# Optimization experiments

Measured on AMD Instinct MI355X. Metric: run time of the kernel, lower is better.

## Reference

```python
import jax, jax.numpy as jnp
import numpy as np

IN_CH, OUT_CH, KS = 64, 128, 3
GRID, DEG = 8, 3
STRIDE, PAD = 1, 1
SIZE = IN_CH * KS * KS            # 576
NCOEF = GRID + DEG                # 11
GRID_RANGE = (-1.0, 1.0)


def _xavier_uniform(key, shape):
    fan_out, fan_in = shape
    a = float(np.sqrt(6.0 / (fan_in + fan_out)))
    return jax.random.uniform(key, shape, minval=-a, maxval=a, dtype=jnp.float32)


def setup_inputs() -> dict:
    key = jax.random.key(0)
    k1, k2, k3 = jax.random.split(key, 3)
    x = jax.random.normal(k1, (8, IN_CH, 32, 32), dtype=jnp.float32)
    # non-trainable knot grid, one row per unfolded feature
    knots = jnp.tile(jnp.linspace(GRID_RANGE[0], GRID_RANGE[1], GRID + 1, dtype=jnp.float32)[None, :], (SIZE, 1))
    coeff = 0.1 * jax.random.normal(k2, (OUT_CH, SIZE, NCOEF), dtype=jnp.float32)
    base_weights = _xavier_uniform(k3, (OUT_CH, SIZE))
    spline_weights = jnp.ones((OUT_CH, SIZE), dtype=jnp.float32)
    return {"x": x, "knots": knots, "coeff": coeff,
            "base_weights": base_weights, "spline_weights": spline_weights}


def bspline_basis(x, grid, k):
    # x: (S, P) evaluation points; grid: (S, G+1) knots. Returns (S, G+k, P).
    h = (grid[:, -1:] - grid[:, :1]) / (grid.shape[1] - 1)
    left = grid[:, :1] - h * jnp.arange(k, 0, -1, dtype=x.dtype)
    right = grid[:, -1:] + h * jnp.arange(1, k + 1, dtype=x.dtype)
    g = jnp.concatenate([left, grid, right], axis=1)  # (S, G+1+2k)
    xe = x[:, None, :]
    B = ((xe >= g[:, :-1, None]) & (xe < g[:, 1:, None])).astype(x.dtype)
    for d in range(1, k + 1):  # de Boor recursion over fixed degree
        B = ((xe - g[:, :-(d + 1), None]) / (g[:, d:-1, None] - g[:, :-(d + 1), None]) * B[:, :-1]
             + (g[:, d + 1:, None] - xe) / (g[:, d + 1:, None] - g[:, 1:-d, None]) * B[:, 1:])
    return B


def _unfold(x):
    # torch F.unfold with channel-major (c, kh, kw) feature ordering
    N, C, H, W = x.shape
    xp = jnp.pad(x, ((0, 0), (0, 0), (PAD, PAD), (PAD, PAD)))
    Hp = (H + 2 * PAD - KS) // STRIDE + 1
    Wp = (W + 2 * PAD - KS) // STRIDE + 1
    patches = jnp.stack([xp[:, :, i:i + STRIDE * Hp:STRIDE, j:j + STRIDE * Wp:STRIDE]
                         for i in range(KS) for j in range(KS)], axis=2)  # (N, C, KS*KS, Hp, Wp)
    L = Hp * Wp
    u = patches.reshape(N, SIZE, L)              # (N, size, L)
    u = jnp.transpose(u, (1, 0, 2)).reshape(SIZE, N * L)  # (size, N*L), col = n*L + l
    return u, Hp, Wp


def reference(x, knots, coeff, base_weights, spline_weights):
    N = x.shape[0]
    u, Hp, Wp = _unfold(x)                                   # (size, P)
    base = base_weights @ jax.nn.silu(u)                     # (Cout, P)
    B = bspline_basis(u, knots, DEG)                         # (size, ncoef, P)
    eff = spline_weights[:, :, None] * coeff                 # (Cout, size, ncoef)
    spl = jnp.einsum('csj,sjp->cp', eff, B)                  # (Cout, P)
    out = (base + spl).reshape(OUT_CH, N, Hp, Wp)
    return jnp.transpose(out, (1, 0, 2, 3))                  # (N, Cout, Hp, Wp)
```

## Files before the change

### kernel.cpp

```cpp
#include <hip/hip_runtime.h>


typedef __attribute__((ext_vector_type(8))) short bf16x8;
typedef __attribute__((ext_vector_type(4))) float f32x4;
typedef __attribute__((ext_vector_type(16))) float f32x16;
typedef __attribute__((ext_vector_type(4))) unsigned short u16x4;

#define WSWZ_BYTES 1769472
#define PART_OFF   WSWZ_BYTES

__device__ __forceinline__ short f2bf(float f) {
    union { float f; unsigned u; } c; c.f = f;
    unsigned r = c.u + 0x7fffu + ((c.u >> 16) & 1u);
    return (short)(r >> 16);
}
__device__ __forceinline__ float bf2f(unsigned short u) {
    union { unsigned u; float f; } c; c.u = ((unsigned)u) << 16;
    return c.f;
}

__global__ void kan_weights(const float* __restrict__ coeff,
                            const float* __restrict__ basew,
                            const float* __restrict__ splw,
                            short* __restrict__ Wswz) {
    __shared__ float coeffL[6336];
    __shared__ float basewL[576];
    __shared__ float splwL[576];
    const int co = blockIdx.x;
    const int t  = threadIdx.x;
    const float* crow = coeff + co * 6336;
    for (int i = t; i < 6336; i += 256) coeffL[i] = crow[i];
    for (int i = t; i < 576; i += 256) {
        basewL[i] = basew[co * 576 + i];
        splwL[i]  = splw[co * 576 + i];
    }
    __syncthreads();
    const int cb = co >> 5, lm = co & 31;
    for (int c = t; c < 864; c += 256) {
        int kk16 = c >> 1, kh = c & 1;
        int f  = kk16 / 36;
        int rm = kk16 - f * 36;
        int tap = rm >> 2, q = rm & 3;
        bf16x8 pack;
#pragma unroll
        for (int j = 0; j < 8; ++j) {
            int ci = q * 16 + kh * 8 + j;
            int s  = ci * 9 + tap;
            float v = (f == 0) ? basewL[s] : splwL[s] * coeffL[s * 11 + (f - 1)];
            pack[j] = f2bf(v);
        }
        *(bf16x8*)(Wswz + (size_t)((kk16 * 4 + cb) * 64 + kh * 32 + lm) * 8) = pack;
    }
}

__global__ __launch_bounds__(256, 3)
void kan_gemm(const float* __restrict__ x,
              const short* __restrict__ Wswz,
              float* __restrict__ part) {
    __shared__ unsigned short xs[4 * 64 * 34];
    __shared__ short Bs[2 * 8704];

    const int t  = threadIdx.x;
    const int w  = t >> 6;
    const int l  = t & 63;
    const int ln = l & 31;
    const int kh = l >> 5;

    const int fg    = blockIdx.x >> 7;
    const int ptile = blockIdx.x & 127;
    const int n     = ptile >> 4;
    const int y0    = (ptile & 15) << 1;

#pragma unroll
    for (int it = 0; it < 8; ++it) {
        int cg = t + it * 256;
        int rr = cg >> 9, ci = (cg >> 3) & 63, q = cg & 7;
        int y  = y0 - 1 + rr;
        f32x4 v = {0.f, 0.f, 0.f, 0.f};
        if (y >= 0 && y < 32)
            v = *(const f32x4*)(x + (((n * 64 + ci) * 32 + y) * 32 + q * 4));
        u16x4 p;
        p.x = (unsigned short)f2bf(v.x); p.y = (unsigned short)f2bf(v.y);
        p.z = (unsigned short)f2bf(v.z); p.w = (unsigned short)f2bf(v.w);
        *(u16x4*)&xs[(rr * 64 + ci) * 34 + q * 4] = p;
    }
    __syncthreads();

    const int f0 = fg * 2;
    for (int it = t; it < 1088; it += 256) {
        int rr  = it / 272;
        int rem = it - rr * 272;
        int xp = rem >> 3, cch = rem & 7, c0 = cch << 3;
        bool interior = (xp >= 1 && xp <= 32);
        bf16x8 packs[2];
#pragma unroll
        for (int j = 0; j < 8; ++j) {
            float v = interior ? bf2f(xs[(rr * 64 + c0 + j) * 34 + (xp - 1)]) : 0.f;
            float tt = 4.f * v + 7.f;
            int   i0 = -100;
            float b0 = 0.f, b1 = 0.f, b2 = 0.f, b3 = 0.f;
            if (tt >= 0.f && tt < 14.f) {
                i0 = (int)tt;
                float fr  = tt - (float)i0;
                float omf = 1.f - fr;
                float fr2 = fr * fr, fr3 = fr2 * fr;
                b0 = omf * omf * omf * (1.f / 6.f);
                b1 = (3.f * fr3 - 6.f * fr2 + 4.f) * (1.f / 6.f);
                b2 = (-3.f * fr3 + 3.f * fr2 + 3.f * fr + 1.f) * (1.f / 6.f);
                b3 = fr3 * (1.f / 6.f);
            }
            float silu = 0.f;
            if (f0 == 0)
                silu = v * __builtin_amdgcn_rcpf(1.f + __expf(-v));
#pragma unroll
            for (int p = 0; p < 2; ++p) {
                int f = f0 + p;
                float val;
                if (f == 0) val = silu;
                else {
                    int jj = f - 1;
                    val = 0.f;
                    val = (jj == i0 - 3) ? b0 : val;
                    val = (jj == i0 - 2) ? b1 : val;
                    val = (jj == i0 - 1) ? b2 : val;
                    val = (jj == i0    ) ? b3 : val;
                }
                packs[p][j] = f2bf(val);
            }
        }
        int pix = rr * 34 + xp;
        int swz = (cch ^ (pix & 7)) << 3;
#pragma unroll
        for (int p = 0; p < 2; ++p)
            *(bf16x8*)&Bs[p * 8704 + pix * 64 + swz] = packs[p];
    }
    __syncthreads();

    f32x16 acc[2];
#pragma unroll
    for (int pb = 0; pb < 2; ++pb)
#pragma unroll
        for (int r = 0; r < 16; ++r)
            acc[pb][r] = 0.f;

    const short* Abase = Wswz + (size_t)w * 512 + (size_t)l * 8;
#pragma unroll 1
    for (int p = 0; p < 2; ++p) {
        const short* B0 = Bs + p * 8704;
        const int kbase = (f0 + p) * 36;
#pragma unroll
        for (int q = 0; q < 4; ++q) {
#pragma unroll
            for (int dx = 0; dx < 3; ++dx) {
                bf16x8 a0 = *(const bf16x8*)(Abase + (size_t)(kbase + (0 * 3 + dx) * 4 + q) * 2048);
                bf16x8 a1 = *(const bf16x8*)(Abase + (size_t)(kbase + (1 * 3 + dx) * 4 + q) * 2048);
                bf16x8 a2 = *(const bf16x8*)(Abase + (size_t)(kbase + (2 * 3 + dx) * 4 + q) * 2048);
                const int c = q * 2 + kh;
                bf16x8 b0, b1, b2, b3;
                {
                    int pix0 = 0 * 34 + ln + dx;
                    int pix1 = 1 * 34 + ln + dx;
                    int pix2 = 2 * 34 + ln + dx;
                    int pix3 = 3 * 34 + ln + dx;
                    b0 = *(const bf16x8*)&B0[pix0 * 64 + ((c ^ (pix0 & 7)) << 3)];
                    b1 = *(const bf16x8*)&B0[pix1 * 64 + ((c ^ (pix1 & 7)) << 3)];
                    b2 = *(const bf16x8*)&B0[pix2 * 64 + ((c ^ (pix2 & 7)) << 3)];
                    b3 = *(const bf16x8*)&B0[pix3 * 64 + ((c ^ (pix3 & 7)) << 3)];
                }
                acc[0] = __builtin_amdgcn_mfma_f32_32x32x16_bf16(a0, b0, acc[0], 0, 0, 0);
                acc[1] = __builtin_amdgcn_mfma_f32_32x32x16_bf16(a0, b1, acc[1], 0, 0, 0);
                acc[0] = __builtin_amdgcn_mfma_f32_32x32x16_bf16(a1, b1, acc[0], 0, 0, 0);
                acc[1] = __builtin_amdgcn_mfma_f32_32x32x16_bf16(a1, b2, acc[1], 0, 0, 0);
                acc[0] = __builtin_amdgcn_mfma_f32_32x32x16_bf16(a2, b2, acc[0], 0, 0, 0);
                acc[1] = __builtin_amdgcn_mfma_f32_32x32x16_bf16(a2, b3, acc[1], 0, 0, 0);
            }
        }
    }

    float* dst = part + (size_t)fg * 1048576;
#pragma unroll
    for (int pb = 0; pb < 2; ++pb) {
        int y = y0 + pb;
#pragma unroll
        for (int r = 0; r < 16; ++r) {
            int row = (r & 3) + 8 * (r >> 2) + 4 * kh;
            int co  = w * 32 + row;
            dst[((size_t)(n * 128 + co) * 32 + y) * 32 + ln] = acc[pb][r];
        }
    }
}

__global__ void kan_reduce(const float* __restrict__ part,
                           float* __restrict__ out) {
    const int r = blockIdx.x;
    const int p = r & 127;
    const int i = r >> 7;
    const int n  = p >> 4;
    const int yp = p & 15;
    const int c  = i * 256 + threadIdx.x;
    const int co = c >> 4;
    const int rem = c & 15;
    const int yy = rem >> 3, xq = rem & 7;
    const size_t idx = ((size_t)(n * 128 + co) * 32 + yp * 2 + yy) * 8 + xq;
    f32x4 a = ((const f32x4*)part)[idx];
#pragma unroll
    for (int s = 1; s < 6; ++s)
        a += ((const f32x4*)(part + (size_t)s * 1048576))[idx];
    ((f32x4*)out)[idx] = a;
}

extern "C" void kernel_launch(void* const* d_in, const int* in_sizes, int n_in,
                              void* d_out, int out_size, void* d_ws, size_t ws_size,
                              hipStream_t stream) {
    const float* x     = (const float*)d_in[0];
    const float* coeff = (const float*)d_in[2];
    const float* basew = (const float*)d_in[3];
    const float* splw  = (const float*)d_in[4];
    float* out = (float*)d_out;

    short* Wswz = (short*)d_ws;
    float* part = (float*)((char*)d_ws + PART_OFF);

    kan_weights<<<128, 256, 0, stream>>>(coeff, basew, splw, Wswz);
    kan_gemm<<<768, 256, 0, stream>>>(x, Wswz, part);
    kan_reduce<<<1024, 256, 0, stream>>>(part, out);
}
```

Measured before the change: 111.7 us.

## Precompute basis tiles once in prep kernel and stream them to LDS in GEMM

Moves the unfold, SiLU and B-spline basis evaluation out of the GEMM into the prep kernel. There it is computed once per pixel tile for all 12 feature groups and written to a ~27MB bf16 workspace, in the same swizzled layout the GEMM's LDS expects. Before, each of the 6 feature-group blocks recomputed the x tile and its basis. The GEMM now only copies its precomputed tile into LDS with global_load_lds, drops the xs buffer, and raises launch bounds to 4 waves per SIMD. The cost is extra global write and read traffic for the Phi buffer, plus a prep kernel with fewer, heavier blocks.

```diff
diff --git a/kernel.cpp b/kernel.cpp
--- a/kernel.cpp
+++ b/kernel.cpp
@@ -7,7 +7,9 @@
 typedef __attribute__((ext_vector_type(4))) unsigned short u16x4;
 
 #define WSWZ_BYTES 1769472
-#define PART_OFF   WSWZ_BYTES
+#define PHI_OFF    WSWZ_BYTES
+#define PHI_BYTES  26738688
+#define PART_OFF   (PHI_OFF + PHI_BYTES)
 
 __device__ __forceinline__ short f2bf(float f) {
     union { float f; unsigned u; } c; c.f = f;
@@ -19,45 +21,114 @@
     return c.f;
 }
 
-__global__ void kan_weights(const float* __restrict__ coeff,
-                            const float* __restrict__ basew,
-                            const float* __restrict__ splw,
-                            short* __restrict__ Wswz) {
+__global__ void kan_prep(const float* __restrict__ coeff,
+                         const float* __restrict__ basew,
+                         const float* __restrict__ splw,
+                         const float* __restrict__ x,
+                         short* __restrict__ Wswz,
+                         short* __restrict__ Phi) {
     __shared__ float coeffL[6336];
     __shared__ float basewL[576];
     __shared__ float splwL[576];
-    const int co = blockIdx.x;
-    const int t  = threadIdx.x;
-    const float* crow = coeff + co * 6336;
-    for (int i = t; i < 6336; i += 256) coeffL[i] = crow[i];
-    for (int i = t; i < 576; i += 256) {
-        basewL[i] = basew[co * 576 + i];
-        splwL[i]  = splw[co * 576 + i];
-    }
-    __syncthreads();
-    const int cb = co >> 5, lm = co & 31;
-    for (int c = t; c < 864; c += 256) {
-        int kk16 = c >> 1, kh = c & 1;
-        int f  = kk16 / 36;
-        int rm = kk16 - f * 36;
-        int tap = rm >> 2, q = rm & 3;
-        bf16x8 pack;
-#pragma unroll
-        for (int j = 0; j < 8; ++j) {
-            int ci = q * 16 + kh * 8 + j;
-            int s  = ci * 9 + tap;
-            float v = (f == 0) ? basewL[s] : splwL[s] * coeffL[s * 11 + (f - 1)];
-            pack[j] = f2bf(v);
-        }
-        *(bf16x8*)(Wswz + (size_t)((kk16 * 4 + cb) * 64 + kh * 32 + lm) * 8) = pack;
-    }
-}
-
-__global__ __launch_bounds__(256, 3)
-void kan_gemm(const float* __restrict__ x,
+    __shared__ unsigned short xs[4 * 64 * 34];
+    const int t = threadIdx.x;
+
+    if (blockIdx.x < 128) {
+        const int co = blockIdx.x;
+        const float* crow = coeff + co * 6336;
+        for (int i = t; i < 6336; i += 256) coeffL[i] = crow[i];
+        for (int i = t; i < 576; i += 256) {
+            basewL[i] = basew[co * 576 + i];
+            splwL[i]  = splw[co * 576 + i];
+        }
+        __syncthreads();
+        const int cb = co >> 5, lm = co & 31;
+        for (int c = t; c < 864; c += 256) {
+            int kk16 = c >> 1, kh = c & 1;
+            int f  = kk16 / 36;
+            int rm = kk16 - f * 36;
+            int tap = rm >> 2, q = rm & 3;
+            bf16x8 pack;
+#pragma unroll
+            for (int j = 0; j < 8; ++j) {
+                int ci = q * 16 + kh * 8 + j;
+                int s  = ci * 9 + tap;
+                float v = (f == 0) ? basewL[s] : splwL[s] * coeffL[s * 11 + (f - 1)];
+                pack[j] = f2bf(v);
+            }
+            *(bf16x8*)(Wswz + (size_t)((kk16 * 4 + cb) * 64 + kh * 32 + lm) * 8) = pack;
+        }
+    } else {
+        const int ptile = blockIdx.x - 128;
+        const int n     = ptile >> 4;
+        const int y0    = (ptile & 15) << 1;
+
+#pragma unroll
+        for (int it = 0; it < 8; ++it) {
+            int cg = t + it * 256;
+            int rr = cg >> 9, ci = (cg >> 3) & 63, q = cg & 7;
+            int y  = y0 - 1 + rr;
+            f32x4 v = {0.f, 0.f, 0.f, 0.f};
+            if (y >= 0 && y < 32)
+                v = *(const f32x4*)(x + (((n * 64 + ci) * 32 + y) * 32 + q * 4));
+            u16x4 p;
+            p.x = (unsigned short)f2bf(v.x); p.y = (unsigned short)f2bf(v.y);
+            p.z = (unsigned short)f2bf(v.z); p.w = (unsigned short)f2bf(v.w);
+            *(u16x4*)&xs[(rr * 64 + ci) * 34 + q * 4] = p;
+        }
+        __syncthreads();
+
+        for (int it = t; it < 1088; it += 256) {
+            int rr  = it / 272;
+            int rem = it - rr * 272;
+            int xp = rem >> 3, cch = rem & 7, c0 = cch << 3;
+            bool interior = (xp >= 1 && xp <= 32);
+            bf16x8 packs[12];
+#pragma unroll
+            for (int j = 0; j < 8; ++j) {
+                float v = interior ? bf2f(xs[(rr * 64 + c0 + j) * 34 + (xp - 1)]) : 0.f;
+                float tt = 4.f * v + 7.f;
+                int   i0 = -100;
+                float b0 = 0.f, b1 = 0.f, b2 = 0.f, b3 = 0.f;
+                if (tt >= 0.f && tt < 14.f) {
+                    i0 = (int)tt;
+                    float fr  = tt - (float)i0;
+                    float omf = 1.f - fr;
+                    float fr2 = fr * fr, fr3 = fr2 * fr;
+                    b0 = omf * omf * omf * (1.f / 6.f);
+                    b1 = (3.f * fr3 - 6.f * fr2 + 4.f) * (1.f / 6.f);
+                    b2 = (-3.f * fr3 + 3.f * fr2 + 3.f * fr + 1.f) * (1.f / 6.f);
+                    b3 = fr3 * (1.f / 6.f);
+                }
+                float silu = v * __builtin_amdgcn_rcpf(1.f + __expf(-v));
+                packs[0][j] = f2bf(silu);
+#pragma unroll
+                for (int f = 1; f < 12; ++f) {
+                    int jj = f - 1;
+                    float val = 0.f;
+                    val = (jj == i0 - 3) ? b0 : val;
+                    val = (jj == i0 - 2) ? b1 : val;
+                    val = (jj == i0 - 1) ? b2 : val;
+                    val = (jj == i0    ) ? b3 : val;
+                    packs[f][j] = f2bf(val);
+                }
+            }
+            int pix = rr * 34 + xp;
+            int swz = (cch ^ (pix & 7)) << 3;
+#pragma unroll
+            for (int f = 0; f < 12; ++f) {
+                int fg = f >> 1, pl = f & 1;
+                *(bf16x8*)&Phi[((size_t)(fg * 128 + ptile) * 2 + pl) * 8704 + pix * 64 + swz]
+                    = packs[f];
+            }
+        }
+    }
+}
+
+__global__ __launch_bounds__(256, 4)
+void kan_gemm(const short* __restrict__ Phi,
               const short* __restrict__ Wswz,
               float* __restrict__ part) {
-    __shared__ unsigned short xs[4 * 64 * 34];
     __shared__ short Bs[2 * 8704];
 
     const int t  = threadIdx.x;
@@ -71,68 +142,11 @@
     const int n     = ptile >> 4;
     const int y0    = (ptile & 15) << 1;
 
-#pragma unroll
-    for (int it = 0; it < 8; ++it) {
-        int cg = t + it * 256;
-        int rr = cg >> 9, ci = (cg >> 3) & 63, q = cg & 7;
-        int y  = y0 - 1 + rr;
-        f32x4 v = {0.f, 0.f, 0.f, 0.f};
-        if (y >= 0 && y < 32)
-            v = *(const f32x4*)(x + (((n * 64 + ci) * 32 + y) * 32 + q * 4));
-        u16x4 p;
-        p.x = (unsigned short)f2bf(v.x); p.y = (unsigned short)f2bf(v.y);
-        p.z = (unsigned short)f2bf(v.z); p.w = (unsigned short)f2bf(v.w);
-        *(u16x4*)&xs[(rr * 64 + ci) * 34 + q * 4] = p;
-    }
-    __syncthreads();
-
-    const int f0 = fg * 2;
-    for (int it = t; it < 1088; it += 256) {
-        int rr  = it / 272;
-        int rem = it - rr * 272;
-        int xp = rem >> 3, cch = rem & 7, c0 = cch << 3;
-        bool interior = (xp >= 1 && xp <= 32);
-        bf16x8 packs[2];
-#pragma unroll
-        for (int j = 0; j < 8; ++j) {
-            float v = interior ? bf2f(xs[(rr * 64 + c0 + j) * 34 + (xp - 1)]) : 0.f;
-            float tt = 4.f * v + 7.f;
-            int   i0 = -100;
-            float b0 = 0.f, b1 = 0.f, b2 = 0.f, b3 = 0.f;
-            if (tt >= 0.f && tt < 14.f) {
-                i0 = (int)tt;
-                float fr  = tt - (float)i0;
-                float omf = 1.f - fr;
-                float fr2 = fr * fr, fr3 = fr2 * fr;
-                b0 = omf * omf * omf * (1.f / 6.f);
-                b1 = (3.f * fr3 - 6.f * fr2 + 4.f) * (1.f / 6.f);
-                b2 = (-3.f * fr3 + 3.f * fr2 + 3.f * fr + 1.f) * (1.f / 6.f);
-                b3 = fr3 * (1.f / 6.f);
-            }
-            float silu = 0.f;
-            if (f0 == 0)
-                silu = v * __builtin_amdgcn_rcpf(1.f + __expf(-v));
-#pragma unroll
-            for (int p = 0; p < 2; ++p) {
-                int f = f0 + p;
-                float val;
-                if (f == 0) val = silu;
-                else {
-                    int jj = f - 1;
-                    val = 0.f;
-                    val = (jj == i0 - 3) ? b0 : val;
-                    val = (jj == i0 - 2) ? b1 : val;
-                    val = (jj == i0 - 1) ? b2 : val;
-                    val = (jj == i0    ) ? b3 : val;
-                }
-                packs[p][j] = f2bf(val);
-            }
-        }
-        int pix = rr * 34 + xp;
-        int swz = (cch ^ (pix & 7)) << 3;
-#pragma unroll
-        for (int p = 0; p < 2; ++p)
-            *(bf16x8*)&Bs[p * 8704 + pix * 64 + swz] = packs[p];
+    const char* src = (const char*)Phi + (size_t)(fg * 128 + ptile) * 34816;
+    for (int i = t; i < 2176; i += 256) {
+        auto gsrc = (const __attribute__((address_space(1))) unsigned int*)(src + (size_t)i * 16);
+        auto ldst = (__attribute__((address_space(3))) unsigned int*)((char*)&Bs[0] + i * 16);
+        __builtin_amdgcn_global_load_lds(gsrc, ldst, 16, 0, 0);
     }
     __syncthreads();
 
@@ -147,7 +161,7 @@
 #pragma unroll 1
     for (int p = 0; p < 2; ++p) {
         const short* B0 = Bs + p * 8704;
-        const int kbase = (f0 + p) * 36;
+        const int kbase = (fg * 2 + p) * 36;
 #pragma unroll
         for (int q = 0; q < 4; ++q) {
 #pragma unroll
@@ -219,9 +233,10 @@
     float* out = (float*)d_out;
 
     short* Wswz = (short*)d_ws;
+    short* Phi  = (short*)((char*)d_ws + PHI_OFF);
     float* part = (float*)((char*)d_ws + PART_OFF);
 
-    kan_weights<<<128, 256, 0, stream>>>(coeff, basew, splw, Wswz);
-    kan_gemm<<<768, 256, 0, stream>>>(x, Wswz, part);
+    kan_prep<<<256, 256, 0, stream>>>(coeff, basew, splw, x, Wswz, Phi);
+    kan_gemm<<<768, 256, 0, stream>>>(Phi, Wswz, part);
     kan_reduce<<<1024, 256, 0, stream>>>(part, out);
 }
```

Result: slower. 123.9 us (+10.9%).
